# Kernel optimization log

Hardware: AMD Instinct MI355X
Metric: run time of the kernel (lower is better)

The kernel has to match this reference:

```python
import jax, jax.numpy as jnp
import numpy as np

TOPK_FRAC = 0.05  # init arg `topk` (fraction of pool kept)


def setup_inputs() -> dict:
    key = jax.random.key(0)
    k1, k2 = jax.random.split(key)
    x = jax.random.normal(k1, (16, 256, 32, 32), dtype=jnp.float32)
    # nn.Parameter(torch.rand(P, C)) -> uniform [0, 1)
    visual_concept_pool = jax.random.uniform(k2, (2048, 256), dtype=jnp.float32)
    return {"x": x, "visual_concept_pool": visual_concept_pool}


def reference(x, visual_concept_pool):
    n, c, h, w = x.shape
    P = visual_concept_pool.shape[0]
    L = h * w
    xf = x.reshape(n, c, L)                              # [n, c, L]
    # dot_product[n, P, L] = pool @ xf
    dot = jnp.einsum('pc,ncl->npl', visual_concept_pool, xf)
    pool_norm = jnp.sqrt(jnp.sum(visual_concept_pool ** 2, axis=1))   # [P]
    x_norm = jnp.sqrt(jnp.sum(xf ** 2, axis=1))                        # [n, L]
    cos = dot / (pool_norm[None, :, None] * x_norm[:, None, :])       # [n, P, L]

    # mode 1.1: top-k over the pool dimension per (n, pixel)
    keep = int(TOPK_FRAC * P)
    cos_t = jnp.transpose(cos, (0, 2, 1))                # [n, L, P]
    _, idx = jax.lax.top_k(jnp.abs(cos_t), keep)         # [n, L, keep]
    mask = jnp.zeros_like(cos_t).at[
        jnp.arange(n)[:, None, None],
        jnp.arange(L)[None, :, None],
        idx,
    ].set(1.0)                                           # [n, L, P]
    masked = cos_t * mask
    normed = masked / jnp.sum(masked, axis=-1, keepdims=True)  # renormalize over P
    # reconstruct[n, c, L] = pool^T @ cos
    recon = jnp.einsum('pc,nlp->ncl', visual_concept_pool, normed)
    return recon.reshape(n, c, h, w)
```

## Files before the change

kernel.cpp:

```cpp
#include <hip/hip_runtime.h>
#include <hip/hip_fp16.h>

typedef unsigned short u16;
typedef _Float16 half8 __attribute__((ext_vector_type(8)));
typedef float floatx4 __attribute__((ext_vector_type(4)));

#define C_DIM 256
#define P_DIM 2048
#define L_DIM 1024
#define N_DIM 16
#define KEEP 102
#define KPAD 104
#define QTR_PIX 4096
#define SCALE 256.0f

__device__ __forceinline__ void st8(u16* dst, const u16* s) {
  uint4 u;
  u.x = (unsigned)s[0] | ((unsigned)s[1] << 16);
  u.y = (unsigned)s[2] | ((unsigned)s[3] << 16);
  u.z = (unsigned)s[4] | ((unsigned)s[5] << 16);
  u.w = (unsigned)s[6] | ((unsigned)s[7] << 16);
  *(uint4*)dst = u;
}

__device__ __forceinline__ u16 f2h_ftz(float v) {
  if (fabsf(v) < 6.103515625e-5f) return 0;
  return __half_as_ushort(__float2half(v));
}

__device__ __forceinline__ void gl_lds16(const u16* g, u16* l) {
  __builtin_amdgcn_global_load_lds(
      (const __attribute__((address_space(1))) unsigned int*)g,
      (__attribute__((address_space(3))) unsigned int*)l, 16, 0, 0);
}

union SMem {
  u16 sB[2][2][8][512];
  struct { float tbuf[8][260]; int2 kpw[8][KPAD]; } sel;
};

__global__ __launch_bounds__(256) void k_pinv(const float* __restrict__ pool,
                                              float* __restrict__ pinv) {
  int p = blockIdx.x * 256 + threadIdx.x;
  const float4* row = (const float4*)(pool + (size_t)p * C_DIM);
  float s = 0.f;
#pragma unroll
  for (int i = 0; i < C_DIM / 4; ++i) {
    float4 v = row[i];
    s += v.x * v.x + v.y * v.y + v.z * v.z + v.w * v.w;
  }
  pinv[p] = 1.0f / sqrtf(s);
}

__device__ __forceinline__ void packpool_body(int b,
                                              const float* __restrict__ pool,
                                              const float* __restrict__ pinv,
                                              u16* __restrict__ ah,
                                              u16* __restrict__ al,
                                              u16* __restrict__ ph) {
  int tid = b * 512 + threadIdx.x;
  int lane = tid & 63;
  int ks = (tid >> 6) & 7;
  int pm = tid >> 9;
  int p = pm * 16 + (lane & 15);
  int c0 = ks * 32 + ((lane >> 4) << 3);
  float sc = pinv[p] * SCALE;
  const float* src = pool + (size_t)p * C_DIM + c0;
  u16 h8[8], l8[8], p8[8];
#pragma unroll
  for (int j = 0; j < 8; ++j) {
    float raw = src[j];
    p8[j] = __half_as_ushort(__float2half(raw));
    float v = raw * sc;
    u16 h = f2h_ftz(v);
    float r = v - __half2float(__ushort_as_half(h));
    h8[j] = h;
    l8[j] = f2h_ftz(r);
  }
  size_t o = (size_t)tid * 8;
  st8(ah + o, h8); st8(al + o, l8);
  st8(ph + (size_t)p * C_DIM + c0, p8);
}

__device__ __forceinline__ void packx_body(int pb, int pq,
                                           const float* __restrict__ x,
                                           u16* __restrict__ xh,
                                           u16* __restrict__ xl) {
  int t = threadIdx.x;
  int lane = t & 63;
  int ks = (t >> 6) & 7;
  int pn = pq * 256 + pb;
  int pix = pn * 16 + (lane & 15);
  int n = pix >> 10, l = pix & 1023;
  int c0 = ks * 32 + ((lane >> 4) << 3);
  const float* src = x + ((size_t)(n * C_DIM + c0)) * L_DIM + l;
  u16 h8[8], l8[8];
#pragma unroll
  for (int j = 0; j < 8; ++j) {
    float v = src[(size_t)j * L_DIM] * SCALE;
    u16 h = f2h_ftz(v);
    float r = v - __half2float(__ushort_as_half(h));
    h8[j] = h;
    l8[j] = f2h_ftz(r);
  }
  size_t o = ((size_t)pn * 512 + (size_t)ks * 64 + lane) * 8;
  st8(xh + o, h8); st8(xl + o, l8);
}

__global__ __launch_bounds__(512) void k_pre(const float* __restrict__ pool,
                                             const float* __restrict__ pinv,
                                             u16* __restrict__ ah,
                                             u16* __restrict__ al,
                                             u16* __restrict__ ph,
                                             const float* __restrict__ x,
                                             u16* __restrict__ xh,
                                             u16* __restrict__ xl) {
  int b = blockIdx.x;
  if (b < 128) packpool_body(b, pool, pinv, ah, al, ph);
  else packx_body(b - 128, 0, x, xh, xl);
}

__device__ __forceinline__ void mfma_body(int b, int mq,
                                          const u16* __restrict__ ah_,
                                          const u16* __restrict__ al_,
                                          const u16* __restrict__ xh_,
                                          const u16* __restrict__ xl_,
                                          float* __restrict__ sbuf,
                                          u16 (*sB)[2][8][512]) {
  const int t = threadIdx.x, lane = t & 63, w = t >> 6;
  const int pT = b & 15, pixT = b >> 4;
  const int pm = pT * 8 + w;
  const int pnBase = mq * 256 + pixT * 8;
  const half8* A8h = (const half8*)ah_;
  const half8* A8l = (const half8*)al_;
  const u16* xsrc[2] = {xh_, xl_};

  floatx4 acc[8];
#pragma unroll
  for (int nt = 0; nt < 8; ++nt) acc[nt] = (floatx4){0.f, 0.f, 0.f, 0.f};

#pragma unroll
  for (int q = 0; q < 2; ++q) {
    int id = w * 2 + q;
    int arr = id >> 3, nt = id & 7;
    gl_lds16(xsrc[arr] + ((size_t)(pnBase + nt) * 512 + lane) * 8,
             &sB[0][arr][nt][0]);
  }
  __syncthreads();

#pragma unroll 1
  for (int ks = 0; ks < 8; ++ks) {
    const int cur = ks & 1;
    half8 aH, aL;
    {
      size_t idx = (size_t)pm * 512 + (size_t)ks * 64 + lane;
      aH = A8h[idx]; aL = A8l[idx];
    }
    if (ks < 7) {
#pragma unroll
      for (int q = 0; q < 2; ++q) {
        int id = w * 2 + q;
        int arr = id >> 3, nt = id & 7;
        gl_lds16(xsrc[arr] + ((size_t)(pnBase + nt) * 512 + (ks + 1) * 64 + lane) * 8,
                 &sB[cur ^ 1][arr][nt][0]);
      }
    }
#pragma unroll
    for (int nt = 0; nt < 8; ++nt) {
      half8 bh = *(const half8*)&sB[cur][0][nt][lane * 8];
      half8 bl = *(const half8*)&sB[cur][1][nt][lane * 8];
      floatx4 c = acc[nt];
      c = __builtin_amdgcn_mfma_f32_16x16x32_f16(aH, bh, c, 0, 0, 0);
      c = __builtin_amdgcn_mfma_f32_16x16x32_f16(aH, bl, c, 0, 0, 0);
      c = __builtin_amdgcn_mfma_f32_16x16x32_f16(aL, bh, c, 0, 0, 0);
      acc[nt] = c;
    }
    __syncthreads();
  }

  const int qr = lane >> 4, cl = lane & 15;
  const int pix0 = pixT * 128;
  const int pcol = pT * 128 + w * 16;
#pragma unroll
  for (int nt = 0; nt < 8; ++nt) {
    float* dst = sbuf + (size_t)(pix0 + nt * 16 + cl) * P_DIM + pcol + qr * 4;
    *(float4*)dst = make_float4(acc[nt][0], acc[nt][1], acc[nt][2], acc[nt][3]);
  }
}

__device__ __forceinline__ void select_body(int b, int sq,
                                            const float* __restrict__ sbuf,
                                            const u16* __restrict__ pool_h,
                                            float* __restrict__ out,
                                            float (*tbuf)[260],
                                            int2 (*kpw)[KPAD]) {
  const int t = threadIdx.x;
  const int lane = t & 63;
  const int wv = t >> 6;
  const int gp0 = sq * QTR_PIX + b * 8;
  const int n = gp0 >> 10;
  const int l0 = gp0 & 1023;
  const float* sp = sbuf + (size_t)(b * 8 + wv) * P_DIM;

  float4 v[8];
#pragma unroll
  for (int q = 0; q < 8; ++q) v[q] = *(const float4*)(sp + q * 256 + lane * 4);

  if (lane < KPAD - KEEP) kpw[wv][KEEP + lane] = make_int2(0, 0);

  float M = 0.f;
#pragma unroll
  for (int q = 0; q < 8; ++q) {
    M = fmaxf(M, fabsf(v[q].x)); M = fmaxf(M, fabsf(v[q].y));
    M = fmaxf(M, fabsf(v[q].z)); M = fmaxf(M, fabsf(v[q].w));
  }
#pragma unroll
  for (int off = 1; off < 64; off <<= 1) M = fmaxf(M, __shfl_xor(M, off));
  const unsigned bitsM = __float_as_uint(M);

  auto countGE = [&](float mf) -> unsigned {
    unsigned cnt = 0;
#pragma unroll
    for (int q = 0; q < 8; ++q) {
      cnt += (unsigned)__popcll(__ballot(fabsf(v[q].x) >= mf));
      cnt += (unsigned)__popcll(__ballot(fabsf(v[q].y) >= mf));
      cnt += (unsigned)__popcll(__ballot(fabsf(v[q].z) >= mf));
      cnt += (unsigned)__popcll(__ballot(fabsf(v[q].w) >= mf));
    }
    return cnt;
  };

  const unsigned t1 = (bitsM > (1u << 23)) ? bitsM - (1u << 23) : 1u;
  const unsigned t2 = (bitsM > (2u << 23)) ? bitsM - (2u << 23) : 1u;
  const unsigned t3 = (bitsM > (3u << 23)) ? bitsM - (3u << 23) : 1u;
  const unsigned t4 = (bitsM > (5u << 23)) ? bitsM - (5u << 23) : 1u;
  const float g1 = __uint_as_float(t1), g2 = __uint_as_float(t2);
  const float g3 = __uint_as_float(t3), g4 = __uint_as_float(t4);
  unsigned c1 = 0, c2 = 0, c3 = 0, c4 = 0;
#pragma unroll
  for (int q = 0; q < 8; ++q) {
    const float* f = (const float*)&v[q];
#pragma unroll
    for (int rr = 0; rr < 4; ++rr) {
      float av = fabsf(f[rr]);
      c1 += (unsigned)__popcll(__ballot(av >= g1));
      c2 += (unsigned)__popcll(__ballot(av >= g2));
      c3 += (unsigned)__popcll(__ballot(av >= g3));
      c4 += (unsigned)__popcll(__ballot(av >= g4));
    }
  }

  unsigned lo = 0u, hi = 1u, cl_ = P_DIM, ch_ = 0u;
  bool exact = false;
  if (c1 == (unsigned)KEEP)      { lo = t1; exact = true; }
  else if (c2 == (unsigned)KEEP) { lo = t2; exact = true; }
  else if (c3 == (unsigned)KEEP) { lo = t3; exact = true; }
  else if (c4 == (unsigned)KEEP) { lo = t4; exact = true; }
  else if (c1 > (unsigned)KEEP)  { lo = t1; cl_ = c1; hi = bitsM + 1u; ch_ = 0u; }
  else if (c2 > (unsigned)KEEP)  { lo = t2; cl_ = c2; hi = t1; ch_ = c1; }
  else if (c3 > (unsigned)KEEP)  { lo = t3; cl_ = c3; hi = t2; ch_ = c2; }
  else if (c4 > (unsigned)KEEP)  { lo = t4; cl_ = c4; hi = t3; ch_ = c3; }
  else                           { lo = 0u; cl_ = P_DIM; hi = t4; ch_ = c4; }

  int it = 0;
  while (!exact && hi - lo > 1u) {
    unsigned span = hi - lo;
    unsigned step;
    if ((it++ & 1) == 0) {
      step = (unsigned)((float)span * (float)(cl_ - KEEP) / (float)(cl_ - ch_));
    } else {
      step = span >> 1;
    }
    if (step < 1u) step = 1u;
    else if (step > span - 1u) step = span - 1u;
    unsigned m = lo + step;
    unsigned cnt = countGE(__uint_as_float(m));
    if (cnt == (unsigned)KEEP) { lo = m; exact = true; break; }
    if (cnt > (unsigned)KEEP) { lo = m; cl_ = cnt; } else { hi = m; ch_ = cnt; }
  }
  const float V = __uint_as_float(lo);
  const float Vp = exact ? V : __uint_as_float(lo + 1u);

  unsigned rrem = 0u;
  if (!exact) {
    unsigned gt = countGE(Vp);
    rrem = (unsigned)KEEP - gt;
  }

  unsigned gmask[8], tmask[8];
#pragma unroll
  for (int q = 0; q < 8; ++q) {
    const float* f = (const float*)&v[q];
    unsigned gm = 0, tm = 0;
#pragma unroll
    for (int rr = 0; rr < 4; ++rr) {
      float av = fabsf(f[rr]);
      if (av >= Vp) gm |= (1u << rr);
      else if (av >= V) tm |= (1u << rr);
    }
    gmask[q] = gm; tmask[q] = tm;
  }

  const unsigned long long lowm = (1ull << lane) - 1ull;
  unsigned base = 0, tiebase = 0;
  float Ssum = 0.f;
#pragma unroll
  for (int q = 0; q < 8; ++q) {
    const float* f = (const float*)&v[q];
    unsigned km = gmask[q];
    if (rrem != 0u) {
      unsigned teq = 0, myeqb = 0;
#pragma unroll
      for (int rr = 0; rr < 4; ++rr) {
        unsigned long long beq = __ballot((tmask[q] >> rr) & 1u);
        teq += (unsigned)__popcll(beq);
        myeqb += (unsigned)__popcll(beq & lowm);
      }
      unsigned cum = 0;
#pragma unroll
      for (int rr = 0; rr < 4; ++rr) {
        if ((tmask[q] >> rr) & 1u) {
          if (tiebase + myeqb + cum < rrem) km |= (1u << rr);
          ++cum;
        }
      }
      tiebase += teq;
    }
    unsigned long long bk[4];
    unsigned tot = 0, myb = 0;
#pragma unroll
    for (int rr = 0; rr < 4; ++rr) {
      bk[rr] = __ballot((km >> rr) & 1u);
      tot += (unsigned)__popcll(bk[rr]);
      myb += (unsigned)__popcll(bk[rr] & lowm);
    }
    {
      unsigned cum = 0;
#pragma unroll
      for (int rr = 0; rr < 4; ++rr) {
        if ((km >> rr) & 1u) {
          unsigned pos = base + myb + cum;
          kpw[wv][pos] = make_int2((q * 256 + lane * 4 + rr) << 9,
                                   __float_as_int(f[rr]));
          Ssum += f[rr];
          ++cum;
        }
      }
    }
    base += tot;
  }

#pragma unroll
  for (int off = 1; off < 64; off <<= 1) Ssum += __shfl_xor(Ssum, off);
  const float invS = 1.0f / Ssum;

  __builtin_amdgcn_wave_barrier();

  float a0 = 0.f, a1 = 0.f, a2 = 0.f, a3 = 0.f;
  const char* pb = (const char*)(pool_h + 4 * lane);
  int2 eA[4], eB[4];
  uint2 rA[4], rB[4];

  auto PROC = [&](const int2* e, const uint2* r) {
#pragma unroll
    for (int j = 0; j < 4; ++j) {
      float w2 = __int_as_float(e[j].y);
      unsigned rx = r[j].x, ry = r[j].y;
      asm volatile("v_fma_mix_f32 %0, %1, %2, %0 op_sel:[0,0,0] op_sel_hi:[0,1,0]"
                   : "+v"(a0) : "v"(w2), "v"(rx));
      asm volatile("v_fma_mix_f32 %0, %1, %2, %0 op_sel:[0,1,0] op_sel_hi:[0,1,0]"
                   : "+v"(a1) : "v"(w2), "v"(rx));
      asm volatile("v_fma_mix_f32 %0, %1, %2, %0 op_sel:[0,0,0] op_sel_hi:[0,1,0]"
                   : "+v"(a2) : "v"(w2), "v"(ry));
      asm volatile("v_fma_mix_f32 %0, %1, %2, %0 op_sel:[0,1,0] op_sel_hi:[0,1,0]"
                   : "+v"(a3) : "v"(w2), "v"(ry));
    }
  };

#pragma unroll
  for (int j = 0; j < 4; ++j) eA[j] = kpw[wv][j];
#pragma unroll
  for (int j = 0; j < 4; ++j)
    rA[j] = *(const uint2*)(pb + (unsigned)eA[j].x);

#pragma unroll 1
  for (int k = 0; k < KPAD; k += 8) {
    const int kb = k + 4;
#pragma unroll
    for (int j = 0; j < 4; ++j) eB[j] = kpw[wv][kb + j];
#pragma unroll
    for (int j = 0; j < 4; ++j)
      rB[j] = *(const uint2*)(pb + (unsigned)eB[j].x);
    PROC(eA, rA);
    const int ka = (k + 8 < KPAD) ? k + 8 : 0;
#pragma unroll
    for (int j = 0; j < 4; ++j) eA[j] = kpw[wv][ka + j];
#pragma unroll
    for (int j = 0; j < 4; ++j)
      rA[j] = *(const uint2*)(pb + (unsigned)eA[j].x);
    PROC(eB, rB);
  }
  a0 *= invS; a1 *= invS; a2 *= invS; a3 *= invS;

  *(float4*)&tbuf[wv][4 * lane] = make_float4(a0, a1, a2, a3);
  __syncthreads();

  {
    int c = t >> 1, lq = t & 1;
    float4 o = make_float4(tbuf[4 * lq + 0][c], tbuf[4 * lq + 1][c],
                           tbuf[4 * lq + 2][c], tbuf[4 * lq + 3][c]);
    *(float4*)(out + ((size_t)(n * C_DIM + c)) * L_DIM + l0 + 4 * lq) = o;
  }
}

__global__ __launch_bounds__(512, 4) void k_main(const u16* __restrict__ ah_,
                                                 const u16* __restrict__ al_,
                                                 const u16* __restrict__ xh_,
                                                 const u16* __restrict__ xl_,
                                                 const u16* __restrict__ ph,
                                                 const float* __restrict__ x,
                                                 float* __restrict__ sbuf0,
                                                 float* __restrict__ sbuf1,
                                                 float* __restrict__ out,
                                                 int mq, int sq, int pq) {
  __shared__ __align__(16) SMem sm;
  const int b = blockIdx.x;
  const int nsel = (sq >= 0) ? 512 : 0;
  const int npk = (pq >= 0) ? 256 : 0;
  if (b < nsel) {
    select_body(b, sq, (sq & 1) ? sbuf1 : sbuf0, ph, out, sm.sel.tbuf, sm.sel.kpw);
  } else if (b < nsel + npk) {
    packx_body(b - nsel, pq, x, (u16*)xh_, (u16*)xl_);
  } else {
    mfma_body(b - nsel - npk, mq, ah_, al_, xh_, xl_, (mq & 1) ? sbuf1 : sbuf0, sm.sB);
  }
}

extern "C" void kernel_launch(void* const* d_in, const int* in_sizes, int n_in,
                              void* d_out, int out_size, void* d_ws, size_t ws_size,
                              hipStream_t stream) {
  const float* x = (const float*)d_in[0];
  const float* pool = (const float*)d_in[1];
  float* out = (float*)d_out;
  char* wsb = (char*)d_ws;
  float* sbuf0 = (float*)wsb;
  float* sbuf1 = (float*)(wsb + 33554432);
  u16* xh = (u16*)(wsb + 67108864);
  u16* xl = xh + 4194304;
  u16* ah = xl + 4194304;
  u16* al = ah + 524288;
  u16* ph = al + 524288;
  float* pinv = (float*)(ph + 524288);

  k_pinv<<<P_DIM / 256, 256, 0, stream>>>(pool, pinv);
  k_pre<<<384, 512, 0, stream>>>(pool, pinv, ah, al, ph, x, xh, xl);

  k_main<<<768, 512, 0, stream>>>(ah, al, xh, xl, ph, x, sbuf0, sbuf1, out, 0, -1, 1);
  k_main<<<1280, 512, 0, stream>>>(ah, al, xh, xl, ph, x, sbuf0, sbuf1, out, 1, 0, 2);
  k_main<<<1280, 512, 0, stream>>>(ah, al, xh, xl, ph, x, sbuf0, sbuf1, out, 2, 1, 3);
  k_main<<<1024, 512, 0, stream>>>(ah, al, xh, xl, ph, x, sbuf0, sbuf1, out, 3, 2, -1);
  k_main<<<512, 512, 0, stream>>>(ah, al, xh, xl, ph, x, sbuf0, sbuf1, out, -1, 3, -1);
}
```

Baseline: 249.1 us.

## Replace staged multi-launch pipeline with persistent flag-synchronized kernel

Five phase-staggered k_main launches are replaced by one persistent k_pipe kernel of 1024 blocks. Half the blocks run the MFMA phase and the other half run selection. They coordinate through global atomic counters, so each group starts as soon as its own dependencies are ready rather than waiting at launch boundaries. The pre-kernel now packs two quarters of x up front, and the MFMA blocks pack the remaining quarters. This removes kernel launch gaps and global barriers but depends on all blocks being co-resident to avoid deadlock, and it adds spin-wait overhead.

```diff
diff --git a/kernel.cpp b/kernel.cpp
--- a/kernel.cpp
+++ b/kernel.cpp
@@ -36,12 +36,35 @@
 
 union SMem {
   u16 sB[2][2][8][512];
-  struct { float tbuf[8][260]; int2 kpw[8][KPAD]; } sel;
+  struct {
+    float tbuf[8][260];
+    int2  kpw[8][KPAD];
+  } sel;
 };
 
+#define F_PACK 0
+#define F_MF   128
+#define F_RD   256
+#define F_TOTAL 384
+
+__device__ __forceinline__ void wait_flag(int* f, int target) {
+  if (threadIdx.x == 0) {
+    while (__hip_atomic_load(f, __ATOMIC_RELAXED, __HIP_MEMORY_SCOPE_AGENT) < target)
+      __builtin_amdgcn_s_sleep(8);
+    (void)__hip_atomic_load(f, __ATOMIC_ACQUIRE, __HIP_MEMORY_SCOPE_AGENT);
+  }
+  __syncthreads();
+}
+__device__ __forceinline__ void signal_flag(int* f) {
+  if (threadIdx.x == 0)
+    __hip_atomic_fetch_add(f, 1, __ATOMIC_RELEASE, __HIP_MEMORY_SCOPE_AGENT);
+}
+
 __global__ __launch_bounds__(256) void k_pinv(const float* __restrict__ pool,
-                                              float* __restrict__ pinv) {
+                                              float* __restrict__ pinv,
+                                              int* __restrict__ flags) {
   int p = blockIdx.x * 256 + threadIdx.x;
+  if (p < F_TOTAL) flags[p] = 0;
   const float4* row = (const float4*)(pool + (size_t)p * C_DIM);
   float s = 0.f;
 #pragma unroll
@@ -117,7 +140,8 @@
                                              u16* __restrict__ xl) {
   int b = blockIdx.x;
   if (b < 128) packpool_body(b, pool, pinv, ah, al, ph);
-  else packx_body(b - 128, 0, x, xh, xl);
+  else if (b < 384) packx_body(b - 128, 0, x, xh, xl);
+  else packx_body(b - 384, 1, x, xh, xl);
 }
 
 __device__ __forceinline__ void mfma_body(int b, int mq,
@@ -380,24 +404,20 @@
 #pragma unroll
   for (int j = 0; j < 4; ++j) eA[j] = kpw[wv][j];
 #pragma unroll
-  for (int j = 0; j < 4; ++j)
-    rA[j] = *(const uint2*)(pb + (unsigned)eA[j].x);
-
+  for (int j = 0; j < 4; ++j) rA[j] = *(const uint2*)(pb + (unsigned)eA[j].x);
 #pragma unroll 1
   for (int k = 0; k < KPAD; k += 8) {
     const int kb = k + 4;
 #pragma unroll
     for (int j = 0; j < 4; ++j) eB[j] = kpw[wv][kb + j];
 #pragma unroll
-    for (int j = 0; j < 4; ++j)
-      rB[j] = *(const uint2*)(pb + (unsigned)eB[j].x);
+    for (int j = 0; j < 4; ++j) rB[j] = *(const uint2*)(pb + (unsigned)eB[j].x);
     PROC(eA, rA);
     const int ka = (k + 8 < KPAD) ? k + 8 : 0;
 #pragma unroll
     for (int j = 0; j < 4; ++j) eA[j] = kpw[wv][ka + j];
 #pragma unroll
-    for (int j = 0; j < 4; ++j)
-      rA[j] = *(const uint2*)(pb + (unsigned)eA[j].x);
+    for (int j = 0; j < 4; ++j) rA[j] = *(const uint2*)(pb + (unsigned)eA[j].x);
     PROC(eB, rB);
   }
   a0 *= invS; a1 *= invS; a2 *= invS; a3 *= invS;
@@ -413,26 +433,51 @@
   }
 }
 
-__global__ __launch_bounds__(512, 4) void k_main(const u16* __restrict__ ah_,
+__global__ __launch_bounds__(512, 4) void k_pipe(const u16* __restrict__ ah_,
                                                  const u16* __restrict__ al_,
-                                                 const u16* __restrict__ xh_,
-                                                 const u16* __restrict__ xl_,
+                                                 u16* __restrict__ xh_,
+                                                 u16* __restrict__ xl_,
                                                  const u16* __restrict__ ph,
                                                  const float* __restrict__ x,
                                                  float* __restrict__ sbuf0,
                                                  float* __restrict__ sbuf1,
                                                  float* __restrict__ out,
-                                                 int mq, int sq, int pq) {
+                                                 int* __restrict__ flags) {
   __shared__ __align__(16) SMem sm;
   const int b = blockIdx.x;
-  const int nsel = (sq >= 0) ? 512 : 0;
-  const int npk = (pq >= 0) ? 256 : 0;
-  if (b < nsel) {
-    select_body(b, sq, (sq & 1) ? sbuf1 : sbuf0, ph, out, sm.sel.tbuf, sm.sel.kpw);
-  } else if (b < nsel + npk) {
-    packx_body(b - nsel, pq, x, (u16*)xh_, (u16*)xl_);
+  const int g = b >> 5;
+  const int r = b & 31;
+  int* pack_cnt = flags + F_PACK;
+  int* mf_cnt = flags + F_MF;
+  int* rd_cnt = flags + F_RD;
+
+  if (r < 16) {
+    const int mb = r + 16 * g;
+#pragma unroll 1
+    for (int q = 0; q < 4; ++q) {
+      if (q >= 2) {
+        wait_flag(&rd_cnt[(q - 2) * 32 + g], 16);
+        wait_flag(&pack_cnt[q * 32 + g], 8);
+      }
+      mfma_body(mb, q, ah_, al_, xh_, xl_, (q & 1) ? sbuf1 : sbuf0, sm.sB);
+      __syncthreads();
+      signal_flag(&mf_cnt[q * 32 + g]);
+      if (q < 2 && r < 8) {
+        packx_body(8 * g + r, q + 2, x, xh_, xl_);
+        __syncthreads();
+        signal_flag(&pack_cnt[(q + 2) * 32 + g]);
+      }
+    }
   } else {
-    mfma_body(b - nsel - npk, mq, ah_, al_, xh_, xl_, (mq & 1) ? sbuf1 : sbuf0, sm.sB);
+    const int sb = g * 16 + (r - 16);
+#pragma unroll 1
+    for (int q = 0; q < 4; ++q) {
+      wait_flag(&mf_cnt[q * 32 + g], 16);
+      select_body(sb, q, (q & 1) ? sbuf1 : sbuf0, ph, out,
+                  sm.sel.tbuf, sm.sel.kpw);
+      __syncthreads();
+      signal_flag(&rd_cnt[q * 32 + g]);
+    }
   }
 }
 
@@ -451,13 +496,9 @@
   u16* al = ah + 524288;
   u16* ph = al + 524288;
   float* pinv = (float*)(ph + 524288);
-
-  k_pinv<<<P_DIM / 256, 256, 0, stream>>>(pool, pinv);
-  k_pre<<<384, 512, 0, stream>>>(pool, pinv, ah, al, ph, x, xh, xl);
-
-  k_main<<<768, 512, 0, stream>>>(ah, al, xh, xl, ph, x, sbuf0, sbuf1, out, 0, -1, 1);
-  k_main<<<1280, 512, 0, stream>>>(ah, al, xh, xl, ph, x, sbuf0, sbuf1, out, 1, 0, 2);
-  k_main<<<1280, 512, 0, stream>>>(ah, al, xh, xl, ph, x, sbuf0, sbuf1, out, 2, 1, 3);
-  k_main<<<1024, 512, 0, stream>>>(ah, al, xh, xl, ph, x, sbuf0, sbuf1, out, 3, 2, -1);
-  k_main<<<512, 512, 0, stream>>>(ah, al, xh, xl, ph, x, sbuf0, sbuf1, out, -1, 3, -1);
-}
+  int* flags = (int*)(pinv + 2048);
+
+  k_pinv<<<P_DIM / 256, 256, 0, stream>>>(pool, pinv, flags);
+  k_pre<<<640, 512, 0, stream>>>(pool, pinv, ah, al, ph, x, xh, xl);
+  k_pipe<<<1024, 512, 0, stream>>>(ah, al, xh, xl, ph, x, sbuf0, sbuf1, out, flags);
+}
```

Result: slower. 458.3 us (+84.0%).
